# Performance work log

Measured on AMD Instinct MI355X. Metric: run time of the kernel, lower is better.

The kernel has to match this reference:

```python
import jax, jax.numpy as jnp
import numpy as np

T, H, I, E, TOPK = 2048, 2048, 1408, 8, 2


def setup_inputs() -> dict:
    key = jax.random.key(0)
    k1, k2, k3, k4 = jax.random.split(key, 4)
    x = jax.random.normal(k1, (T, H), dtype=jnp.float32)
    router_logits = jax.random.normal(k2, (T, E), dtype=jnp.float32)
    # scale weights down so activations stay well-conditioned
    w13_weight = jax.random.normal(k3, (E, 2 * I, H), dtype=jnp.float32) * (1.0 / np.sqrt(H))
    w2_weight = jax.random.normal(k4, (E, H, I), dtype=jnp.float32) * (1.0 / np.sqrt(I))
    return {"x": x, "router_logits": router_logits, "w13_weight": w13_weight,
            "w2_weight": w2_weight, "top_k": TOPK}


def reference(x, router_logits, w13_weight, w2_weight, top_k):
    # --- select_experts: softmax scoring, top-k, renormalize ---
    probs = jax.nn.softmax(router_logits.astype(jnp.float32), axis=-1)   # [T, E]
    topk_w, topk_ids = jax.lax.top_k(probs, top_k)                        # [T, k]
    topk_w = topk_w / jnp.sum(topk_w, axis=-1, keepdims=True)             # renormalize
    topk_w = topk_w.astype(x.dtype)

    n_tok = x.shape[0]
    n_exp = w13_weight.shape[0]
    inter = w2_weight.shape[2]

    # dense combine weights [T, E]: zero for unselected experts
    comb = jnp.zeros((n_tok, n_exp), dtype=x.dtype)
    comb = comb.at[jnp.arange(n_tok)[:, None], topk_ids].add(topk_w)

    # --- fused_experts: gated SiLU MLP per expert, weighted combine ---
    gate_up = jnp.einsum('th,eih->tei', x, w13_weight)                    # [T, E, 2I]
    gate, up = gate_up[..., :inter], gate_up[..., inter:]
    act = jax.nn.silu(gate) * up                                          # [T, E, I]
    out = jnp.einsum('tei,ehi,te->th', act, w2_weight, comb)              # [T, H]
    return out
```

## Files before the change

kernel.cpp:

```cpp
#include <hip/hip_runtime.h>
#include <hip/hip_bf16.h>
#include <stdint.h>

#define T_TOK 2048
#define H_DIM 2048
#define I_DIM 1408
#define NEXP  8
#define NPOS  4096
#define NPAD  5120
#define MAXT  40

typedef short short8 __attribute__((ext_vector_type(8)));
typedef float f32x4  __attribute__((ext_vector_type(4)));

__device__ __forceinline__ short f2bf(float f) {
  union { float f; uint32_t u; } v; v.f = f;
  uint32_t r = (v.u + 0x7FFFu + ((v.u >> 16) & 1u)) >> 16;
  return (short)r;
}

__device__ __forceinline__ short8 cvt8(f32x4 a, f32x4 b) {
  __hip_bfloat162 h0 = __float22bfloat162_rn(float2{a[0], a[1]});
  __hip_bfloat162 h1 = __float22bfloat162_rn(float2{a[2], a[3]});
  __hip_bfloat162 h2 = __float22bfloat162_rn(float2{b[0], b[1]});
  __hip_bfloat162 h3 = __float22bfloat162_rn(float2{b[2], b[3]});
  short2 s0, s1, s2, s3;
  __builtin_memcpy(&s0, &h0, 4); __builtin_memcpy(&s1, &h1, 4);
  __builtin_memcpy(&s2, &h2, 4); __builtin_memcpy(&s3, &h3, 4);
  short8 r;
  r[0] = s0.x; r[1] = s0.y; r[2] = s1.x; r[3] = s1.y;
  r[4] = s2.x; r[5] = s2.y; r[6] = s3.x; r[7] = s3.y;
  return r;
}

__device__ __forceinline__ void load_lds16(const void* g, void* l) {
  __builtin_amdgcn_global_load_lds((const __attribute__((address_space(1))) uint32_t*)g,
                                   (__attribute__((address_space(3))) uint32_t*)l,
                                   16, 0, 0);
}

__global__ void k_routing(const float* __restrict__ logits,
                          int* __restrict__ pos_token,
                          float* __restrict__ pos_w,
                          int* __restrict__ eoff,
                          int* __restrict__ inv) {
  __shared__ int   s_ids[T_TOK];
  __shared__ float s_w0[T_TOK];
  __shared__ float s_w1[T_TOK];
  __shared__ int s_cnt[NEXP], s_cur[NEXP], s_off[NEXP + 1];
  const int tid = threadIdx.x;
  if (tid < NEXP) { s_cnt[tid] = 0; s_cur[tid] = 0; }
  for (int p = tid; p < NPAD; p += blockDim.x) { pos_token[p] = 0; pos_w[p] = 0.f; }
  __syncthreads();

  for (int t = tid; t < T_TOK; t += blockDim.x) {
    float l[NEXP];
#pragma unroll
    for (int e = 0; e < NEXP; ++e) l[e] = logits[t * NEXP + e];
    int b0 = 0; float v0 = l[0];
#pragma unroll
    for (int e = 1; e < NEXP; ++e) if (l[e] > v0) { v0 = l[e]; b0 = e; }
    int b1 = -1; float v1 = -1e30f;
#pragma unroll
    for (int e = 0; e < NEXP; ++e) if (e != b0 && l[e] > v1) { v1 = l[e]; b1 = e; }
    float t1 = __expf(v1 - v0);
    float w0 = 1.f / (1.f + t1);
    float w1 = 1.f - w0;
    s_ids[t] = b0 | (b1 << 8);
    s_w0[t] = w0; s_w1[t] = w1;
    atomicAdd(&s_cnt[b0], 1);
    atomicAdd(&s_cnt[b1], 1);
  }
  __syncthreads();
  if (tid == 0) {
    int acc = 0;
    for (int e = 0; e < NEXP; ++e) {
      s_off[e] = acc;
      acc += (s_cnt[e] + 127) & ~127;
    }
    s_off[NEXP] = acc;
    for (int e = 0; e <= NEXP; ++e) eoff[e] = s_off[e];
  }
  __syncthreads();
  for (int t = tid; t < T_TOK; t += blockDim.x) {
    int ids = s_ids[t];
    int e0 = ids & 255, e1 = ids >> 8;
    int p0 = s_off[e0] + atomicAdd(&s_cur[e0], 1);
    pos_token[p0] = t; pos_w[p0] = s_w0[t];
    int p1 = s_off[e1] + atomicAdd(&s_cur[e1], 1);
    pos_token[p1] = t; pos_w[p1] = s_w1[t];
    inv[2 * t] = p0; inv[2 * t + 1] = p1;
  }
}

__global__ void k_gather(const float* __restrict__ x,
                         const int* __restrict__ pos_token,
                         short* __restrict__ xg) {
  const int p = blockIdx.x;
  const int tid = threadIdx.x;
  const int tok = pos_token[p];
  const float4* src = (const float4*)(x + (size_t)tok * H_DIM);
  float4 a = src[tid * 2];
  float4 b = src[tid * 2 + 1];
  short8 s;
  s[0] = f2bf(a.x); s[1] = f2bf(a.y); s[2] = f2bf(a.z); s[3] = f2bf(a.w);
  s[4] = f2bf(b.x); s[5] = f2bf(b.y); s[6] = f2bf(b.z); s[7] = f2bf(b.w);
  ((short8*)(xg + (size_t)p * H_DIM))[tid] = s;
}

__device__ __forceinline__ int tile_expert(const int* eoff, int row0) {
  int e = 0;
#pragma unroll
  for (int i = 1; i < NEXP; ++i) if (row0 >= eoff[i]) e = i;
  return e;
}

__global__ __launch_bounds__(256, 3) void k_gateup(
    const short* __restrict__ xg, const float* __restrict__ w13,
    const int* __restrict__ eoff, short* __restrict__ act) {
  __shared__ __align__(16) short a_s[2][128 * 32];
  __shared__ __align__(16) short bg_s[2][64 * 32];
  __shared__ __align__(16) short bu_s[2][64 * 32];

  int bxr = blockIdx.x;
  const int bx = (bxr & 7) * 110 + (bxr >> 3);
  const int tile = bx / 22;
  const int nt = bx - tile * 22;
  const int row0 = tile * 128;
  if (row0 >= eoff[NEXP]) return;
  const int e = tile_expert(eoff, row0);

  const int tid = threadIdx.x;
  const int wid = tid >> 6;
  const int lane = tid & 63;
  const int wm = wid >> 1, wn = wid & 1;

  f32x4 accg[4][2] = {};
  f32x4 accu[4][2] = {};

  const short* aG  = xg + (size_t)row0 * H_DIM;
  const float* bgG = w13 + (size_t)e * (2 * I_DIM) * H_DIM + (size_t)(nt * 64) * H_DIM;
  const float* buG = bgG + (size_t)I_DIM * H_DIM;

  const int row  = tid >> 2;
  const int scol = ((tid & 3) ^ ((tid >> 3) & 3)) * 8;

  auto stageA = [&](int t, int bi) {
    const int ks = t * 32;
    load_lds16(aG + (size_t)row * H_DIM + ks + scol,        (char*)a_s[bi] + wid * 1024);
    load_lds16(aG + (size_t)(64 + row) * H_DIM + ks + scol, (char*)a_s[bi] + 4096 + wid * 1024);
  };

  f32x4 g0, g1, u0, u1;
  auto ldB = [&](int t) {
    const int ks = t * 32;
    const float* sg = bgG + (size_t)row * H_DIM + ks + scol;
    const float* su = buG + (size_t)row * H_DIM + ks + scol;
    g0 = *(const f32x4*)sg; g1 = *(const f32x4*)(sg + 4);
    u0 = *(const f32x4*)su; u1 = *(const f32x4*)(su + 4);
  };
  auto wrB = [&](int bi) {
    *(short8*)((char*)bg_s[bi] + tid * 16) = cvt8(g0, g1);
    *(short8*)((char*)bu_s[bi] + tid * 16) = cvt8(u0, u1);
  };

  auto compute = [&](int bi) {
    const int asl = ((lane >> 4) ^ ((lane >> 1) & 3)) * 16;
    short8 af[4];
#pragma unroll
    for (int fm = 0; fm < 4; ++fm) {
      int m = wm * 64 + fm * 16 + (lane & 15);
      af[fm] = *(const short8*)((const char*)a_s[bi] + m * 64 + asl);
    }
#pragma unroll
    for (int fn = 0; fn < 2; ++fn) {
      int n = wn * 32 + fn * 16 + (lane & 15);
      short8 bg = *(const short8*)((const char*)bg_s[bi] + n * 64 + asl);
      short8 bu = *(const short8*)((const char*)bu_s[bi] + n * 64 + asl);
#pragma unroll
      for (int fm = 0; fm < 4; ++fm)
        accg[fm][fn] = __builtin_amdgcn_mfma_f32_16x16x32_bf16(af[fm], bg, accg[fm][fn], 0, 0, 0);
#pragma unroll
      for (int fm = 0; fm < 4; ++fm)
        accu[fm][fn] = __builtin_amdgcn_mfma_f32_16x16x32_bf16(af[fm], bu, accu[fm][fn], 0, 0, 0);
    }
  };

  const int NK = H_DIM / 32;
  stageA(0, 0); ldB(0); wrB(0);
  __syncthreads();
  for (int t = 0; t < NK; ++t) {
    int bi = t & 1;
    if (t + 1 < NK) { stageA(t + 1, bi ^ 1); ldB(t + 1); }
    compute(bi);
    if (t + 1 < NK) wrB(bi ^ 1);
    __syncthreads();
  }

#pragma unroll
  for (int fm = 0; fm < 4; ++fm) {
#pragma unroll
    for (int rr = 0; rr < 4; ++rr) {
      int m = wm * 64 + fm * 16 + (lane >> 4) * 4 + rr;
      size_t grow = (size_t)(row0 + m);
#pragma unroll
      for (int fn = 0; fn < 2; ++fn) {
        int col = nt * 64 + wn * 32 + fn * 16 + (lane & 15);
        float g = accg[fm][fn][rr];
        float u = accu[fm][fn][rr];
        float a = g / (1.f + __expf(-g)) * u;
        act[grow * I_DIM + col] = f2bf(a);
      }
    }
  }
}

__global__ __launch_bounds__(256, 3) void k_down(
    const short* __restrict__ act, const float* __restrict__ w2,
    const int* __restrict__ eoff, float* __restrict__ y) {
  __shared__ __align__(16) short a_s[2][128 * 32];
  __shared__ __align__(16) short b_s[2][128 * 32];

  int bxr = blockIdx.x;
  const int bx = (bxr & 7) * 80 + (bxr >> 3);
  const int tile = bx >> 4;
  const int nt = bx & 15;
  const int row0 = tile * 128;
  if (row0 >= eoff[NEXP]) return;
  const int e = tile_expert(eoff, row0);

  const int tid = threadIdx.x;
  const int wid = tid >> 6;
  const int lane = tid & 63;
  const int wm = wid >> 1, wn = wid & 1;

  f32x4 acc[4][4] = {};

  const short* aG = act + (size_t)row0 * I_DIM;
  const float* bG = w2 + (size_t)e * H_DIM * I_DIM + (size_t)(nt * 128) * I_DIM;

  const int row  = tid >> 2;
  const int scol = ((tid & 3) ^ ((tid >> 3) & 3)) * 8;

  auto stageA = [&](int t, int bi) {
    const int ks = t * 32;
    load_lds16(aG + (size_t)row * I_DIM + ks + scol,        (char*)a_s[bi] + wid * 1024);
    load_lds16(aG + (size_t)(64 + row) * I_DIM + ks + scol, (char*)a_s[bi] + 4096 + wid * 1024);
  };

  f32x4 b00, b01, b10, b11;
  auto ldB = [&](int t) {
    const int ks = t * 32;
    const float* s0 = bG + (size_t)row * I_DIM + ks + scol;
    const float* s1 = bG + (size_t)(64 + row) * I_DIM + ks + scol;
    b00 = *(const f32x4*)s0; b01 = *(const f32x4*)(s0 + 4);
    b10 = *(const f32x4*)s1; b11 = *(const f32x4*)(s1 + 4);
  };
  auto wrB = [&](int bi) {
    *(short8*)((char*)b_s[bi] + tid * 16)        = cvt8(b00, b01);
    *(short8*)((char*)b_s[bi] + 4096 + tid * 16) = cvt8(b10, b11);
  };

  auto compute = [&](int bi) {
    const int asl = ((lane >> 4) ^ ((lane >> 1) & 3)) * 16;
    short8 af[4];
#pragma unroll
    for (int fm = 0; fm < 4; ++fm) {
      int m = wm * 64 + fm * 16 + (lane & 15);
      af[fm] = *(const short8*)((const char*)a_s[bi] + m * 64 + asl);
    }
#pragma unroll
    for (int fn = 0; fn < 4; ++fn) {
      int n = wn * 64 + fn * 16 + (lane & 15);
      short8 bb = *(const short8*)((const char*)b_s[bi] + n * 64 + asl);
#pragma unroll
      for (int fm = 0; fm < 4; ++fm)
        acc[fm][fn] = __builtin_amdgcn_mfma_f32_16x16x32_bf16(af[fm], bb, acc[fm][fn], 0, 0, 0);
    }
  };

  const int NK = I_DIM / 32;
  stageA(0, 0); ldB(0); wrB(0);
  __syncthreads();
  for (int t = 0; t < NK; ++t) {
    int bi = t & 1;
    if (t + 1 < NK) { stageA(t + 1, bi ^ 1); ldB(t + 1); }
    compute(bi);
    if (t + 1 < NK) wrB(bi ^ 1);
    __syncthreads();
  }

#pragma unroll
  for (int fm = 0; fm < 4; ++fm) {
#pragma unroll
    for (int rr = 0; rr < 4; ++rr) {
      int m = wm * 64 + fm * 16 + (lane >> 4) * 4 + rr;
      size_t grow = (size_t)(row0 + m);
#pragma unroll
      for (int fn = 0; fn < 4; ++fn) {
        int col = nt * 128 + wn * 64 + fn * 16 + (lane & 15);
        y[grow * H_DIM + col] = acc[fm][fn][rr];
      }
    }
  }
}

__global__ void k_combine(const float* __restrict__ y,
                          const int* __restrict__ inv,
                          const float* __restrict__ pos_w,
                          float* __restrict__ out) {
  const int t = blockIdx.x;
  const int tid = threadIdx.x;
  const int p0 = inv[2 * t], p1 = inv[2 * t + 1];
  const float w0 = pos_w[p0], w1 = pos_w[p1];
  const float4* y0 = (const float4*)(y + (size_t)p0 * H_DIM);
  const float4* y1 = (const float4*)(y + (size_t)p1 * H_DIM);
  float4* o = (float4*)(out + (size_t)t * H_DIM);
#pragma unroll
  for (int i = 0; i < 2; ++i) {
    float4 a = y0[tid * 2 + i];
    float4 b = y1[tid * 2 + i];
    float4 r;
    r.x = w0 * a.x + w1 * b.x;
    r.y = w0 * a.y + w1 * b.y;
    r.z = w0 * a.z + w1 * b.z;
    r.w = w0 * a.w + w1 * b.w;
    o[tid * 2 + i] = r;
  }
}

extern "C" void kernel_launch(void* const* d_in, const int* in_sizes, int n_in,
                              void* d_out, int out_size, void* d_ws, size_t ws_size,
                              hipStream_t stream) {
  const float* x      = (const float*)d_in[0];
  const float* logits = (const float*)d_in[1];
  const float* w13    = (const float*)d_in[2];
  const float* w2     = (const float*)d_in[3];
  (void)in_sizes; (void)n_in; (void)out_size; (void)ws_size;
  float* out = (float*)d_out;
  char* ws = (char*)d_ws;

  size_t o = 0;
  auto alloc = [&](size_t bytes) { size_t r = o; o += (bytes + 255) & ~(size_t)255; return r; };
  short* xg        = (short*)(ws + alloc((size_t)NPAD * H_DIM * 2));
  short* act       = (short*)(ws + alloc((size_t)NPAD * I_DIM * 2));
  float* y         = (float*)(ws + alloc((size_t)NPAD * H_DIM * 4));
  int*   pos_token = (int*)  (ws + alloc((size_t)NPAD * 4));
  float* pos_w     = (float*)(ws + alloc((size_t)NPAD * 4));
  int*   inv       = (int*)  (ws + alloc((size_t)T_TOK * 2 * 4));
  int*   eoff      = (int*)  (ws + alloc((NEXP + 1) * 4));

  k_routing<<<1, 1024, 0, stream>>>(logits, pos_token, pos_w, eoff, inv);
  k_gather<<<NPAD, 256, 0, stream>>>(x, pos_token, xg);
  k_gateup<<<MAXT * 22, 256, 0, stream>>>(xg, w13, eoff, act);
  k_down<<<MAXT * 16, 256, 0, stream>>>(act, w2, eoff, y);
  k_combine<<<T_TOK, 256, 0, stream>>>(y, inv, pos_w, out);
}
```

Measured before the change: 220.2 us.

## Pre-cast w13 to bf16 and stage weights into LDS via direct loads

Adds a separate cast kernel that converts the whole fp32 w13 tensor to bf16 in the workspace on every call. The gate/up GEMM then loads weight tiles straight to LDS with global_load_lds, which removes the per-tile register round trip and in-loop conversion. The blockIdx swizzle is also dropped and launch bounds are relaxed from 3 to 2 waves. The trade-off is an extra full pass over w13 (read fp32, write bf16), while each w13 tile is reused by several token tiles in the GEMM.

```diff
diff --git a/kernel.cpp b/kernel.cpp
--- a/kernel.cpp
+++ b/kernel.cpp
@@ -39,6 +39,18 @@
                                    16, 0, 0);
 }
 
+__global__ void k_cast(const float* __restrict__ src, short* __restrict__ dst, long n16) {
+  long i = (long)blockIdx.x * blockDim.x + threadIdx.x;
+  long stride = (long)gridDim.x * blockDim.x;
+  for (; i < n16; i += stride) {
+    const f32x4* s = (const f32x4*)(src + i * 16);
+    f32x4 a = s[0], b = s[1], c = s[2], d = s[3];
+    short8* o = (short8*)dst + i * 2;
+    o[0] = cvt8(a, b);
+    o[1] = cvt8(c, d);
+  }
+}
+
 __global__ void k_routing(const float* __restrict__ logits,
                           int* __restrict__ pos_token,
                           float* __restrict__ pos_w,
@@ -99,13 +111,10 @@
   const int p = blockIdx.x;
   const int tid = threadIdx.x;
   const int tok = pos_token[p];
-  const float4* src = (const float4*)(x + (size_t)tok * H_DIM);
-  float4 a = src[tid * 2];
-  float4 b = src[tid * 2 + 1];
-  short8 s;
-  s[0] = f2bf(a.x); s[1] = f2bf(a.y); s[2] = f2bf(a.z); s[3] = f2bf(a.w);
-  s[4] = f2bf(b.x); s[5] = f2bf(b.y); s[6] = f2bf(b.z); s[7] = f2bf(b.w);
-  ((short8*)(xg + (size_t)p * H_DIM))[tid] = s;
+  const f32x4* src = (const f32x4*)(x + (size_t)tok * H_DIM);
+  f32x4 a = src[tid * 2];
+  f32x4 b = src[tid * 2 + 1];
+  ((short8*)(xg + (size_t)p * H_DIM))[tid] = cvt8(a, b);
 }
 
 __device__ __forceinline__ int tile_expert(const int* eoff, int row0) {
@@ -115,15 +124,14 @@
   return e;
 }
 
-__global__ __launch_bounds__(256, 3) void k_gateup(
-    const short* __restrict__ xg, const float* __restrict__ w13,
+__global__ __launch_bounds__(256, 2) void k_gateup(
+    const short* __restrict__ xg, const short* __restrict__ wb13,
     const int* __restrict__ eoff, short* __restrict__ act) {
   __shared__ __align__(16) short a_s[2][128 * 32];
   __shared__ __align__(16) short bg_s[2][64 * 32];
   __shared__ __align__(16) short bu_s[2][64 * 32];
 
-  int bxr = blockIdx.x;
-  const int bx = (bxr & 7) * 110 + (bxr >> 3);
+  const int bx = blockIdx.x;
   const int tile = bx / 22;
   const int nt = bx - tile * 22;
   const int row0 = tile * 128;
@@ -139,29 +147,18 @@
   f32x4 accu[4][2] = {};
 
   const short* aG  = xg + (size_t)row0 * H_DIM;
-  const float* bgG = w13 + (size_t)e * (2 * I_DIM) * H_DIM + (size_t)(nt * 64) * H_DIM;
-  const float* buG = bgG + (size_t)I_DIM * H_DIM;
+  const short* bgG = wb13 + (size_t)e * (2 * I_DIM) * H_DIM + (size_t)(nt * 64) * H_DIM;
+  const short* buG = bgG + (size_t)I_DIM * H_DIM;
 
   const int row  = tid >> 2;
   const int scol = ((tid & 3) ^ ((tid >> 3) & 3)) * 8;
 
-  auto stageA = [&](int t, int bi) {
+  auto stage = [&](int t, int bi) {
     const int ks = t * 32;
     load_lds16(aG + (size_t)row * H_DIM + ks + scol,        (char*)a_s[bi] + wid * 1024);
     load_lds16(aG + (size_t)(64 + row) * H_DIM + ks + scol, (char*)a_s[bi] + 4096 + wid * 1024);
-  };
-
-  f32x4 g0, g1, u0, u1;
-  auto ldB = [&](int t) {
-    const int ks = t * 32;
-    const float* sg = bgG + (size_t)row * H_DIM + ks + scol;
-    const float* su = buG + (size_t)row * H_DIM + ks + scol;
-    g0 = *(const f32x4*)sg; g1 = *(const f32x4*)(sg + 4);
-    u0 = *(const f32x4*)su; u1 = *(const f32x4*)(su + 4);
-  };
-  auto wrB = [&](int bi) {
-    *(short8*)((char*)bg_s[bi] + tid * 16) = cvt8(g0, g1);
-    *(short8*)((char*)bu_s[bi] + tid * 16) = cvt8(u0, u1);
+    load_lds16(bgG + (size_t)row * H_DIM + ks + scol,       (char*)bg_s[bi] + wid * 1024);
+    load_lds16(buG + (size_t)row * H_DIM + ks + scol,       (char*)bu_s[bi] + wid * 1024);
   };
 
   auto compute = [&](int bi) {
@@ -187,13 +184,12 @@
   };
 
   const int NK = H_DIM / 32;
-  stageA(0, 0); ldB(0); wrB(0);
+  stage(0, 0);
   __syncthreads();
   for (int t = 0; t < NK; ++t) {
     int bi = t & 1;
-    if (t + 1 < NK) { stageA(t + 1, bi ^ 1); ldB(t + 1); }
+    if (t + 1 < NK) stage(t + 1, bi ^ 1);
     compute(bi);
-    if (t + 1 < NK) wrB(bi ^ 1);
     __syncthreads();
   }
 
@@ -340,8 +336,11 @@
   float* out = (float*)d_out;
   char* ws = (char*)d_ws;
 
+  const size_t n_w13 = (size_t)NEXP * 2 * I_DIM * H_DIM;
+
   size_t o = 0;
   auto alloc = [&](size_t bytes) { size_t r = o; o += (bytes + 255) & ~(size_t)255; return r; };
+  short* wb13      = (short*)(ws + alloc(n_w13 * 2));
   short* xg        = (short*)(ws + alloc((size_t)NPAD * H_DIM * 2));
   short* act       = (short*)(ws + alloc((size_t)NPAD * I_DIM * 2));
   float* y         = (float*)(ws + alloc((size_t)NPAD * H_DIM * 4));
@@ -351,8 +350,9 @@
   int*   eoff      = (int*)  (ws + alloc((NEXP + 1) * 4));
 
   k_routing<<<1, 1024, 0, stream>>>(logits, pos_token, pos_w, eoff, inv);
+  k_cast<<<2048, 256, 0, stream>>>(w13, wb13, (long)(n_w13 / 16));
   k_gather<<<NPAD, 256, 0, stream>>>(x, pos_token, xg);
-  k_gateup<<<MAXT * 22, 256, 0, stream>>>(xg, w13, eoff, act);
+  k_gateup<<<MAXT * 22, 256, 0, stream>>>(xg, wb13, eoff, act);
   k_down<<<MAXT * 16, 256, 0, stream>>>(act, w2, eoff, y);
   k_combine<<<T_TOK, 256, 0, stream>>>(y, inv, pos_w, out);
 }
```

New measurement: 241.5 us. 1.1x slower.

## Deepen B-operand prefetch to two tiles ahead with manual waitcnt in MoE GEMMs

Applied to the files above, without the earlier changes.

Both expert GEMM kernels now keep two register sets of fp32 weight tiles in flight, loading B two k-steps ahead of the one being written to LDS. The loop is unrolled by two with explicit sched_barrier, partial vmcnt waits and raw s_barrier instead of __syncthreads. The goal is to hide global weight-load latency behind MFMA work. The trade-off is higher register pressure, which may hurt occupancy, and hand-tuned waitcnt counts that could be wrong. The gather kernel also switches to the packed cvt8 conversion helper.

```diff
diff --git a/kernel.cpp b/kernel.cpp
--- a/kernel.cpp
+++ b/kernel.cpp
@@ -99,13 +99,10 @@
   const int p = blockIdx.x;
   const int tid = threadIdx.x;
   const int tok = pos_token[p];
-  const float4* src = (const float4*)(x + (size_t)tok * H_DIM);
-  float4 a = src[tid * 2];
-  float4 b = src[tid * 2 + 1];
-  short8 s;
-  s[0] = f2bf(a.x); s[1] = f2bf(a.y); s[2] = f2bf(a.z); s[3] = f2bf(a.w);
-  s[4] = f2bf(b.x); s[5] = f2bf(b.y); s[6] = f2bf(b.z); s[7] = f2bf(b.w);
-  ((short8*)(xg + (size_t)p * H_DIM))[tid] = s;
+  const f32x4* src = (const f32x4*)(x + (size_t)tok * H_DIM);
+  f32x4 a = src[tid * 2];
+  f32x4 b = src[tid * 2 + 1];
+  ((short8*)(xg + (size_t)p * H_DIM))[tid] = cvt8(a, b);
 }
 
 __device__ __forceinline__ int tile_expert(const int* eoff, int row0) {
@@ -150,16 +147,14 @@
     load_lds16(aG + (size_t)row * H_DIM + ks + scol,        (char*)a_s[bi] + wid * 1024);
     load_lds16(aG + (size_t)(64 + row) * H_DIM + ks + scol, (char*)a_s[bi] + 4096 + wid * 1024);
   };
-
-  f32x4 g0, g1, u0, u1;
-  auto ldB = [&](int t) {
+  auto ldB = [&](int t, f32x4& g0, f32x4& g1, f32x4& u0, f32x4& u1) {
     const int ks = t * 32;
     const float* sg = bgG + (size_t)row * H_DIM + ks + scol;
     const float* su = buG + (size_t)row * H_DIM + ks + scol;
     g0 = *(const f32x4*)sg; g1 = *(const f32x4*)(sg + 4);
     u0 = *(const f32x4*)su; u1 = *(const f32x4*)(su + 4);
   };
-  auto wrB = [&](int bi) {
+  auto wrB = [&](int bi, f32x4& g0, f32x4& g1, f32x4& u0, f32x4& u1) {
     *(short8*)((char*)bg_s[bi] + tid * 16) = cvt8(g0, g1);
     *(short8*)((char*)bu_s[bi] + tid * 16) = cvt8(u0, u1);
   };
@@ -187,15 +182,35 @@
   };
 
   const int NK = H_DIM / 32;
-  stageA(0, 0); ldB(0); wrB(0);
-  __syncthreads();
-  for (int t = 0; t < NK; ++t) {
-    int bi = t & 1;
-    if (t + 1 < NK) { stageA(t + 1, bi ^ 1); ldB(t + 1); }
-    compute(bi);
-    if (t + 1 < NK) wrB(bi ^ 1);
-    __syncthreads();
-  }
+  f32x4 g0e, g1e, u0e, u1e, g0o, g1o, u0o, u1o;
+
+  stageA(0, 0);
+  ldB(0, g0e, g1e, u0e, u1e);
+  wrB(0, g0e, g1e, u0e, u1e);
+  ldB(1, g0e, g1e, u0e, u1e);
+  ldB(2, g0o, g1o, u0o, u1o);
+  __syncthreads();
+
+#define GU_STEP(T, G0, G1, U0, U1)                                            \
+  {                                                                           \
+    const int t_ = (T);                                                       \
+    const int bi_ = t_ & 1;                                                   \
+    const int tn_ = (t_ + 1 < NK) ? t_ + 1 : NK - 1;                          \
+    const int tf_ = (t_ + 3 < NK) ? t_ + 3 : NK - 1;                          \
+    stageA(tn_, bi_ ^ 1);                                                     \
+    __builtin_amdgcn_sched_barrier(0);                                        \
+    wrB(bi_ ^ 1, G0, G1, U0, U1);                                             \
+    ldB(tf_, G0, G1, U0, U1);                                                 \
+    compute(bi_);                                                             \
+    asm volatile("s_waitcnt vmcnt(4) lgkmcnt(0)" ::: "memory");               \
+    __builtin_amdgcn_s_barrier();                                             \
+  }
+  for (int tp = 0; tp < NK; tp += 2) {
+    GU_STEP(tp,     g0e, g1e, u0e, u1e);
+    GU_STEP(tp + 1, g0o, g1o, u0o, u1o);
+  }
+#undef GU_STEP
+  asm volatile("s_waitcnt vmcnt(0)" ::: "memory");
 
 #pragma unroll
   for (int fm = 0; fm < 4; ++fm) {
@@ -247,16 +262,14 @@
     load_lds16(aG + (size_t)row * I_DIM + ks + scol,        (char*)a_s[bi] + wid * 1024);
     load_lds16(aG + (size_t)(64 + row) * I_DIM + ks + scol, (char*)a_s[bi] + 4096 + wid * 1024);
   };
-
-  f32x4 b00, b01, b10, b11;
-  auto ldB = [&](int t) {
+  auto ldB = [&](int t, f32x4& b00, f32x4& b01, f32x4& b10, f32x4& b11) {
     const int ks = t * 32;
     const float* s0 = bG + (size_t)row * I_DIM + ks + scol;
     const float* s1 = bG + (size_t)(64 + row) * I_DIM + ks + scol;
     b00 = *(const f32x4*)s0; b01 = *(const f32x4*)(s0 + 4);
     b10 = *(const f32x4*)s1; b11 = *(const f32x4*)(s1 + 4);
   };
-  auto wrB = [&](int bi) {
+  auto wrB = [&](int bi, f32x4& b00, f32x4& b01, f32x4& b10, f32x4& b11) {
     *(short8*)((char*)b_s[bi] + tid * 16)        = cvt8(b00, b01);
     *(short8*)((char*)b_s[bi] + 4096 + tid * 16) = cvt8(b10, b11);
   };
@@ -280,15 +293,35 @@
   };
 
   const int NK = I_DIM / 32;
-  stageA(0, 0); ldB(0); wrB(0);
-  __syncthreads();
-  for (int t = 0; t < NK; ++t) {
-    int bi = t & 1;
-    if (t + 1 < NK) { stageA(t + 1, bi ^ 1); ldB(t + 1); }
-    compute(bi);
-    if (t + 1 < NK) wrB(bi ^ 1);
-    __syncthreads();
-  }
+  f32x4 e0, e1, e2, e3, o0, o1, o2, o3;
+
+  stageA(0, 0);
+  ldB(0, e0, e1, e2, e3);
+  wrB(0, e0, e1, e2, e3);
+  ldB(1, e0, e1, e2, e3);
+  ldB(2, o0, o1, o2, o3);
+  __syncthreads();
+
+#define DN_STEP(T, B0, B1, B2, B3)                                            \
+  {                                                                           \
+    const int t_ = (T);                                                       \
+    const int bi_ = t_ & 1;                                                   \
+    const int tn_ = (t_ + 1 < NK) ? t_ + 1 : NK - 1;                          \
+    const int tf_ = (t_ + 3 < NK) ? t_ + 3 : NK - 1;                          \
+    stageA(tn_, bi_ ^ 1);                                                     \
+    __builtin_amdgcn_sched_barrier(0);                                        \
+    wrB(bi_ ^ 1, B0, B1, B2, B3);                                             \
+    ldB(tf_, B0, B1, B2, B3);                                                 \
+    compute(bi_);                                                             \
+    asm volatile("s_waitcnt vmcnt(4) lgkmcnt(0)" ::: "memory");               \
+    __builtin_amdgcn_s_barrier();                                             \
+  }
+  for (int tp = 0; tp < NK; tp += 2) {
+    DN_STEP(tp,     e0, e1, e2, e3);
+    DN_STEP(tp + 1, o0, o1, o2, o3);
+  }
+#undef DN_STEP
+  asm volatile("s_waitcnt vmcnt(0)" ::: "memory");
 
 #pragma unroll
   for (int fm = 0; fm < 4; ++fm) {
```

Measured after the change: 216.0 us. No clear change (-1.9%).

## Split gate-up GEMM into plain GEMM plus separate SiLU kernel with padded rows

Applied to the files above, without the earlier changes.

The fused gate/up GEMM with a SiLU epilogue becomes a plain GEMM over the concatenated 2816-wide weight, writing 128-column tiles of bf16 gate and up values to a new buffer. A new elementwise kernel then applies SiLU(gate)*up to produce the activation. The gathered input rows are padded to a stride of 2080 to reduce LDS or channel conflicts, and the gather now uses the vectorised converter. The intent is a simpler, more uniform GEMM tile, paid for with an extra kernel launch, an extra round trip through global memory for the gate/up buffer, and bf16 rounding of gate and up before the activation.

```diff
diff --git a/kernel.cpp b/kernel.cpp
--- a/kernel.cpp
+++ b/kernel.cpp
@@ -5,10 +5,12 @@
 #define T_TOK 2048
 #define H_DIM 2048
 #define I_DIM 1408
+#define GU_W  2816
 #define NEXP  8
 #define NPOS  4096
 #define NPAD  5120
 #define MAXT  40
+#define XROW  2080
 
 typedef short short8 __attribute__((ext_vector_type(8)));
 typedef float f32x4  __attribute__((ext_vector_type(4)));
@@ -17,6 +19,10 @@
   union { float f; uint32_t u; } v; v.f = f;
   uint32_t r = (v.u + 0x7FFFu + ((v.u >> 16) & 1u)) >> 16;
   return (short)r;
+}
+__device__ __forceinline__ float bf2f(short s) {
+  union { uint32_t u; float f; } v; v.u = ((uint32_t)(uint16_t)s) << 16;
+  return v.f;
 }
 
 __device__ __forceinline__ short8 cvt8(f32x4 a, f32x4 b) {
@@ -99,13 +105,10 @@
   const int p = blockIdx.x;
   const int tid = threadIdx.x;
   const int tok = pos_token[p];
-  const float4* src = (const float4*)(x + (size_t)tok * H_DIM);
-  float4 a = src[tid * 2];
-  float4 b = src[tid * 2 + 1];
-  short8 s;
-  s[0] = f2bf(a.x); s[1] = f2bf(a.y); s[2] = f2bf(a.z); s[3] = f2bf(a.w);
-  s[4] = f2bf(b.x); s[5] = f2bf(b.y); s[6] = f2bf(b.z); s[7] = f2bf(b.w);
-  ((short8*)(xg + (size_t)p * H_DIM))[tid] = s;
+  const f32x4* src = (const f32x4*)(x + (size_t)tok * H_DIM);
+  f32x4 a = src[tid * 2];
+  f32x4 b = src[tid * 2 + 1];
+  ((short8*)(xg + (size_t)p * XROW))[tid] = cvt8(a, b);
 }
 
 __device__ __forceinline__ int tile_expert(const int* eoff, int row0) {
@@ -115,12 +118,11 @@
   return e;
 }
 
-__global__ __launch_bounds__(256, 3) void k_gateup(
+__global__ __launch_bounds__(256, 3) void k_gu(
     const short* __restrict__ xg, const float* __restrict__ w13,
-    const int* __restrict__ eoff, short* __restrict__ act) {
+    const int* __restrict__ eoff, short* __restrict__ gu) {
   __shared__ __align__(16) short a_s[2][128 * 32];
-  __shared__ __align__(16) short bg_s[2][64 * 32];
-  __shared__ __align__(16) short bu_s[2][64 * 32];
+  __shared__ __align__(16) short b_s[2][128 * 32];
 
   int bxr = blockIdx.x;
   const int bx = (bxr & 7) * 110 + (bxr >> 3);
@@ -135,33 +137,31 @@
   const int lane = tid & 63;
   const int wm = wid >> 1, wn = wid & 1;
 
-  f32x4 accg[4][2] = {};
-  f32x4 accu[4][2] = {};
-
-  const short* aG  = xg + (size_t)row0 * H_DIM;
-  const float* bgG = w13 + (size_t)e * (2 * I_DIM) * H_DIM + (size_t)(nt * 64) * H_DIM;
-  const float* buG = bgG + (size_t)I_DIM * H_DIM;
+  f32x4 acc[4][4] = {};
+
+  const short* aG = xg + (size_t)row0 * XROW;
+  const float* bG = w13 + (size_t)e * GU_W * H_DIM + (size_t)(nt * 128) * H_DIM;
 
   const int row  = tid >> 2;
   const int scol = ((tid & 3) ^ ((tid >> 3) & 3)) * 8;
 
   auto stageA = [&](int t, int bi) {
     const int ks = t * 32;
-    load_lds16(aG + (size_t)row * H_DIM + ks + scol,        (char*)a_s[bi] + wid * 1024);
-    load_lds16(aG + (size_t)(64 + row) * H_DIM + ks + scol, (char*)a_s[bi] + 4096 + wid * 1024);
-  };
-
-  f32x4 g0, g1, u0, u1;
+    load_lds16(aG + (size_t)row * XROW + ks + scol,        (char*)a_s[bi] + wid * 1024);
+    load_lds16(aG + (size_t)(64 + row) * XROW + ks + scol, (char*)a_s[bi] + 4096 + wid * 1024);
+  };
+
+  f32x4 b00, b01, b10, b11;
   auto ldB = [&](int t) {
     const int ks = t * 32;
-    const float* sg = bgG + (size_t)row * H_DIM + ks + scol;
-    const float* su = buG + (size_t)row * H_DIM + ks + scol;
-    g0 = *(const f32x4*)sg; g1 = *(const f32x4*)(sg + 4);
-    u0 = *(const f32x4*)su; u1 = *(const f32x4*)(su + 4);
+    const float* s0 = bG + (size_t)row * H_DIM + ks + scol;
+    const float* s1 = bG + (size_t)(64 + row) * H_DIM + ks + scol;
+    b00 = *(const f32x4*)s0; b01 = *(const f32x4*)(s0 + 4);
+    b10 = *(const f32x4*)s1; b11 = *(const f32x4*)(s1 + 4);
   };
   auto wrB = [&](int bi) {
-    *(short8*)((char*)bg_s[bi] + tid * 16) = cvt8(g0, g1);
-    *(short8*)((char*)bu_s[bi] + tid * 16) = cvt8(u0, u1);
+    *(short8*)((char*)b_s[bi] + tid * 16)        = cvt8(b00, b01);
+    *(short8*)((char*)b_s[bi] + 4096 + tid * 16) = cvt8(b10, b11);
   };
 
   auto compute = [&](int bi) {
@@ -173,16 +173,12 @@
       af[fm] = *(const short8*)((const char*)a_s[bi] + m * 64 + asl);
     }
 #pragma unroll
-    for (int fn = 0; fn < 2; ++fn) {
-      int n = wn * 32 + fn * 16 + (lane & 15);
-      short8 bg = *(const short8*)((const char*)bg_s[bi] + n * 64 + asl);
-      short8 bu = *(const short8*)((const char*)bu_s[bi] + n * 64 + asl);
+    for (int fn = 0; fn < 4; ++fn) {
+      int n = wn * 64 + fn * 16 + (lane & 15);
+      short8 bb = *(const short8*)((const char*)b_s[bi] + n * 64 + asl);
 #pragma unroll
       for (int fm = 0; fm < 4; ++fm)
-        accg[fm][fn] = __builtin_amdgcn_mfma_f32_16x16x32_bf16(af[fm], bg, accg[fm][fn], 0, 0, 0);
-#pragma unroll
-      for (int fm = 0; fm < 4; ++fm)
-        accu[fm][fn] = __builtin_amdgcn_mfma_f32_16x16x32_bf16(af[fm], bu, accu[fm][fn], 0, 0, 0);
+        acc[fm][fn] = __builtin_amdgcn_mfma_f32_16x16x32_bf16(af[fm], bb, acc[fm][fn], 0, 0, 0);
     }
   };
 
@@ -204,14 +200,33 @@
       int m = wm * 64 + fm * 16 + (lane >> 4) * 4 + rr;
       size_t grow = (size_t)(row0 + m);
 #pragma unroll
-      for (int fn = 0; fn < 2; ++fn) {
-        int col = nt * 64 + wn * 32 + fn * 16 + (lane & 15);
-        float g = accg[fm][fn][rr];
-        float u = accu[fm][fn][rr];
-        float a = g / (1.f + __expf(-g)) * u;
-        act[grow * I_DIM + col] = f2bf(a);
+      for (int fn = 0; fn < 4; ++fn) {
+        int col = nt * 128 + wn * 64 + fn * 16 + (lane & 15);
+        gu[grow * GU_W + col] = f2bf(acc[fm][fn][rr]);
       }
     }
+  }
+}
+
+__global__ void k_silu(const short* __restrict__ gu, short* __restrict__ act,
+                       int total8) {
+  const int J = I_DIM / 8;
+  int i = blockIdx.x * blockDim.x + threadIdx.x;
+  const int stride = gridDim.x * blockDim.x;
+  for (; i < total8; i += stride) {
+    int p = i / J;
+    int j = i - p * J;
+    const short* base = gu + (size_t)p * GU_W + j * 8;
+    short8 g8 = *(const short8*)base;
+    short8 u8 = *(const short8*)(base + I_DIM);
+    short8 o;
+#pragma unroll
+    for (int k = 0; k < 8; ++k) {
+      float g = bf2f(g8[k]);
+      float u = bf2f(u8[k]);
+      o[k] = f2bf(g / (1.f + __expf(-g)) * u);
+    }
+    *(short8*)(act + (size_t)p * I_DIM + j * 8) = o;
   }
 }
 
@@ -342,7 +357,8 @@
 
   size_t o = 0;
   auto alloc = [&](size_t bytes) { size_t r = o; o += (bytes + 255) & ~(size_t)255; return r; };
-  short* xg        = (short*)(ws + alloc((size_t)NPAD * H_DIM * 2));
+  short* xg        = (short*)(ws + alloc((size_t)NPAD * XROW * 2));
+  short* gu        = (short*)(ws + alloc((size_t)NPAD * GU_W * 2));
   short* act       = (short*)(ws + alloc((size_t)NPAD * I_DIM * 2));
   float* y         = (float*)(ws + alloc((size_t)NPAD * H_DIM * 4));
   int*   pos_token = (int*)  (ws + alloc((size_t)NPAD * 4));
@@ -352,7 +368,8 @@
 
   k_routing<<<1, 1024, 0, stream>>>(logits, pos_token, pos_w, eoff, inv);
   k_gather<<<NPAD, 256, 0, stream>>>(x, pos_token, xg);
-  k_gateup<<<MAXT * 22, 256, 0, stream>>>(xg, w13, eoff, act);
+  k_gu<<<MAXT * 22, 256, 0, stream>>>(xg, w13, eoff, gu);
+  k_silu<<<2048, 256, 0, stream>>>(gu, act, NPAD * (I_DIM / 8));
   k_down<<<MAXT * 16, 256, 0, stream>>>(act, w2, eoff, y);
   k_combine<<<T_TOK, 256, 0, stream>>>(y, inv, pos_w, out);
 }
```

After: 225.6 us. 1.02x slower.
